# Performance work log

Hardware: AMD Instinct MI355X
Metric: run time of the kernel (lower is better)

## Reference

```python
import jax, jax.numpy as jnp
import numpy as np

B, T, C = 2, 2048, 1024
N_HEAD = 16
HEAD_DIM = C // N_HEAD


def setup_inputs() -> dict:
    key = jax.random.key(0)
    k1, k2, k3 = jax.random.split(key, 3)
    s = 1.0 / np.sqrt(C)
    return {
        "x": jax.random.normal(k1, (B, T, C), dtype=jnp.float32),
        "w_qkv": jax.random.normal(k2, (C, 3 * C), dtype=jnp.float32) * s,
        "b_qkv": jnp.zeros((3 * C,), dtype=jnp.float32),
        "w_out": jax.random.normal(k3, (C, C), dtype=jnp.float32) * s,
        "b_out": jnp.zeros((C,), dtype=jnp.float32),
    }


def reference(x, w_qkv, b_qkv, w_out, b_out):
    b, t, c = x.shape
    qkv = x @ w_qkv + b_qkv                                   # [B,T,3C]
    # Faithful to torch: view(B,T,H,3*hd).transpose(1,2) then split last dim
    qkv = qkv.reshape(b, t, N_HEAD, 3 * HEAD_DIM).transpose(0, 2, 1, 3)  # [B,H,T,3hd]
    q, k, v = jnp.split(qkv, 3, axis=-1)                      # each [B,H,T,hd]
    att = jnp.einsum("bhqd,bhkd->bhqk", q, k) / np.sqrt(HEAD_DIM)
    causal = jnp.tril(jnp.ones((t, t), dtype=bool))
    att = jnp.where(causal[None, None], att, -jnp.inf)
    att = jax.nn.softmax(att, axis=-1)                        # dropout p=0 (eval)
    y = jnp.einsum("bhqk,bhkd->bhqd", att, v)                 # [B,H,T,hd]
    y = y.transpose(0, 2, 1, 3).reshape(b, t, c)
    return y @ w_out + b_out
```

## Files before the change

kernel.cpp:

```cpp
#include <hip/hip_runtime.h>


#define T_SEQ 2048
#define C_DIM 1024
#define NH    16
#define HD    64
#define BT    4096

typedef short bf16x8 __attribute__((ext_vector_type(8)));
typedef float floatx4 __attribute__((ext_vector_type(4)));

static __device__ __forceinline__ unsigned short f2bf(float f) {
    union { float f; unsigned u; } v; v.f = f;
    unsigned u = v.u;
    return (unsigned short)((u + 0x7FFFu + ((u >> 16) & 1u)) >> 16);
}

static __device__ __forceinline__ void gl2lds16(const void* g, void* l) {
    __builtin_amdgcn_global_load_lds(
        (const __attribute__((address_space(1))) unsigned int*)g,
        (__attribute__((address_space(3))) unsigned int*)l, 16, 0, 0);
}

__global__ __launch_bounds__(256) void convert_bf16(const float* __restrict__ in,
                                                    unsigned short* __restrict__ out, int n) {
    int i = (blockIdx.x * 256 + threadIdx.x) * 4;
    const int stride = gridDim.x * 1024;
    for (; i < n; i += stride) {
        float4 f = *(const float4*)(in + i);
        ushort4 o;
        o.x = f2bf(f.x); o.y = f2bf(f.y); o.z = f2bf(f.z); o.w = f2bf(f.w);
        *(ushort4*)(out + i) = o;
    }
}

__global__ __launch_bounds__(256) void transpose_bf16(const float* __restrict__ W,
                                                      unsigned short* __restrict__ Wt,
                                                      int K, int N) {
    __shared__ float tile[64][65];
    const int k0 = blockIdx.y << 6;
    const int n0 = blockIdx.x << 6;
    const int rr = threadIdx.x >> 4;
    const int cc = (threadIdx.x & 15) << 2;
#pragma unroll
    for (int i = 0; i < 4; i++) {
        int r = rr + (i << 4);
        *(float4*)&tile[r][cc] = *(const float4*)(W + (size_t)(k0 + r) * N + n0 + cc);
    }
    __syncthreads();
#pragma unroll
    for (int i = 0; i < 4; i++) {
        int nr = rr + (i << 4);
        ushort4 o;
        o.x = f2bf(tile[cc + 0][nr]);
        o.y = f2bf(tile[cc + 1][nr]);
        o.z = f2bf(tile[cc + 2][nr]);
        o.w = f2bf(tile[cc + 3][nr]);
        *(ushort4*)(Wt + (size_t)(n0 + nr) * K + k0 + cc) = o;
    }
}

#define GEMM_CORE(A_, Bt_, K_)                                                      \
    __shared__ short As[128 * 64];                                                  \
    __shared__ short Bs[128 * 64];                                                  \
    const int tid  = threadIdx.x;                                                   \
    const int lane = tid & 63, wave = tid >> 6;                                     \
    const int ln   = lane & 15, quad = lane >> 4;                                   \
    const int wm   = wave & 1,  wn   = wave >> 1;                                   \
    const int row0 = blockIdx.y << 7;                                               \
    const int col0 = blockIdx.x << 7;                                               \
    const int trow = tid >> 3;                                                      \
    const int tcol = (tid & 7) << 3;                                                \
    floatx4 acc[4][4];                                                              \
    _Pragma("unroll")                                                               \
    for (int i = 0; i < 4; i++)                                                     \
        _Pragma("unroll")                                                           \
        for (int j = 0; j < 4; j++) acc[i][j] = (floatx4){0.f, 0.f, 0.f, 0.f};      \
    for (int k0 = 0; k0 < K_; k0 += 64) {                                           \
        _Pragma("unroll")                                                           \
        for (int i = 0; i < 4; i++) {                                               \
            int r = trow + (i << 5);                                                \
            gl2lds16(A_  + (size_t)(row0 + r) * K_ + k0 + tcol, &As[(r << 6) + tcol]); \
            gl2lds16(Bt_ + (size_t)(col0 + r) * K_ + k0 + tcol, &Bs[(r << 6) + tcol]); \
        }                                                                           \
        __syncthreads();                                                            \
        _Pragma("unroll")                                                           \
        for (int half = 0; half < 2; half++) {                                      \
            bf16x8 af[4], bfr[4];                                                   \
            _Pragma("unroll")                                                       \
            for (int t4 = 0; t4 < 4; t4++) {                                        \
                af[t4]  = *(bf16x8*)&As[(((wm << 6) + (t4 << 4) + ln) << 6) + (half << 5) + (quad << 3)]; \
                bfr[t4] = *(bf16x8*)&Bs[(((wn << 6) + (t4 << 4) + ln) << 6) + (half << 5) + (quad << 3)]; \
            }                                                                       \
            _Pragma("unroll")                                                       \
            for (int mt = 0; mt < 4; mt++)                                          \
                _Pragma("unroll")                                                   \
                for (int nt = 0; nt < 4; nt++)                                      \
                    acc[mt][nt] = __builtin_amdgcn_mfma_f32_16x16x32_bf16(af[mt], bfr[nt], acc[mt][nt], 0, 0, 0); \
        }                                                                           \
        __syncthreads();                                                            \
    }

__global__ __launch_bounds__(256) void gemm_qkv(const unsigned short* __restrict__ A,
                                                const unsigned short* __restrict__ Bt,
                                                const float* __restrict__ bias,
                                                unsigned short* __restrict__ qb,
                                                unsigned short* __restrict__ kb,
                                                unsigned short* __restrict__ vt) {
    GEMM_CORE(A, Bt, 1024)
#pragma unroll
    for (int mt = 0; mt < 4; mt++) {
#pragma unroll
        for (int nt = 0; nt < 4; nt++) {
            int n = col0 + (wn << 6) + (nt << 4) + ln;
            int h = n / 192, r = n % 192;
            int sel = r >> 6, d = r & 63;
            float bv = bias[n];
#pragma unroll
            for (int e = 0; e < 4; e++) {
                int m = row0 + (wm << 6) + (mt << 4) + (quad << 2) + e;
                int b = m >> 11, t = m & 2047;
                float val = acc[mt][nt][e] + bv;
                int bh = b * NH + h;
                if (sel == 0)
                    qb[((size_t)bh * T_SEQ + t) * HD + d] = f2bf(val * 0.125f);
                else if (sel == 1)
                    kb[((size_t)bh * T_SEQ + t) * HD + d] = f2bf(val);
                else
                    vt[((size_t)bh * HD + d) * T_SEQ + t] = f2bf(val);
            }
        }
    }
}

__global__ __launch_bounds__(256) void gemm_out(const unsigned short* __restrict__ A,
                                                const unsigned short* __restrict__ Bt,
                                                const float* __restrict__ bias,
                                                float* __restrict__ out) {
    GEMM_CORE(A, Bt, 1024)
    const int N = 1024;
#pragma unroll
    for (int mt = 0; mt < 4; mt++) {
#pragma unroll
        for (int nt = 0; nt < 4; nt++) {
            int n = col0 + (wn << 6) + (nt << 4) + ln;
            float bv = bias[n];
#pragma unroll
            for (int e = 0; e < 4; e++) {
                int m = row0 + (wm << 6) + (mt << 4) + (quad << 2) + e;
                out[(size_t)m * N + n] = acc[mt][nt][e] + bv;
            }
        }
    }
}

__global__ __launch_bounds__(256, 4) void attn(const unsigned short* __restrict__ qb,
                                               const unsigned short* __restrict__ kb,
                                               const unsigned short* __restrict__ vt,
                                               unsigned short* __restrict__ y) {
    __shared__ short Ks[64][72];
    __shared__ short Vs[64][72];
    __shared__ short QP[64][72];
    const int tid  = threadIdx.x;
    const int w    = tid >> 6, lane = tid & 63;
    const int ln   = lane & 15, quad = lane >> 4;
    const int qt   = 31 - (int)blockIdx.x;
    const int bh   = blockIdx.y;
    const size_t base = (size_t)bh * T_SEQ * HD;
    const int q0   = qt << 6;
    const int sb   = q0 + (w << 4);
    const float NEG_INF = -__builtin_inff();

    const int sr = tid >> 3;
    const int sc = (tid & 7) << 3;

    bf16x8 qtmp[2], kreg[2], vreg[2];
#pragma unroll
    for (int i = 0; i < 2; i++) {
        qtmp[i] = *(const bf16x8*)(qb + base + (size_t)(q0 + sr + (i << 5)) * HD + sc);
        kreg[i] = *(const bf16x8*)(kb + base + (size_t)(sr + (i << 5)) * HD + sc);
        vreg[i] = *(const bf16x8*)(vt + base + (size_t)(sr + (i << 5)) * T_SEQ + sc);
    }
#pragma unroll
    for (int i = 0; i < 2; i++) *(bf16x8*)&QP[sr + (i << 5)][sc] = qtmp[i];
    __syncthreads();

    bf16x8 bq0 = *(bf16x8*)&QP[(w << 4) + ln][quad << 3];
    bf16x8 bq1 = *(bf16x8*)&QP[(w << 4) + ln][32 + (quad << 3)];

    floatx4 o[4];
#pragma unroll
    for (int nt = 0; nt < 4; nt++) o[nt] = (floatx4){0.f, 0.f, 0.f, 0.f};
    float m_prev = NEG_INF, l_run = 0.f;

    for (int kt = 0; kt <= qt; kt++) {
        const int k0 = kt << 6;
        __syncthreads();
#pragma unroll
        for (int i = 0; i < 2; i++) {
            *(bf16x8*)&Ks[sr + (i << 5)][sc] = kreg[i];
            *(bf16x8*)&Vs[sr + (i << 5)][sc] = vreg[i];
        }
        __syncthreads();
        if (kt < qt) {
            const int kn = k0 + 64;
#pragma unroll
            for (int i = 0; i < 2; i++) {
                kreg[i] = *(const bf16x8*)(kb + base + (size_t)(kn + sr + (i << 5)) * HD + sc);
                vreg[i] = *(const bf16x8*)(vt + base + (size_t)(sr + (i << 5)) * T_SEQ + kn + sc);
            }
        }

        const bool diag  = (kt == qt);
        const int  nlive = diag ? w : 3;

        floatx4 st[4];
#pragma unroll
        for (int ktl = 0; ktl < 4; ktl++) {
            if (ktl <= nlive) {
                bf16x8 a0 = *(bf16x8*)&Ks[(ktl << 4) + ln][quad << 3];
                bf16x8 a1 = *(bf16x8*)&Ks[(ktl << 4) + ln][32 + (quad << 3)];
                floatx4 acc = (floatx4){0.f, 0.f, 0.f, 0.f};
                acc = __builtin_amdgcn_mfma_f32_16x16x32_bf16(a0, bq0, acc, 0, 0, 0);
                acc = __builtin_amdgcn_mfma_f32_16x16x32_bf16(a1, bq1, acc, 0, 0, 0);
                st[ktl] = acc;
            }
        }
        if (diag) {
#pragma unroll
            for (int ktl = 0; ktl < 4; ktl++) {
                if (ktl <= nlive) {
#pragma unroll
                    for (int e = 0; e < 4; e++) {
                        int kg = k0 + (ktl << 4) + (quad << 2) + e;
                        if (kg > sb + ln) st[ktl][e] = NEG_INF;
                    }
                }
            }
        }

        float mx = NEG_INF;
#pragma unroll
        for (int ktl = 0; ktl < 4; ktl++)
            if (ktl <= nlive) {
#pragma unroll
                for (int e = 0; e < 4; e++) mx = fmaxf(mx, st[ktl][e]);
            }
        mx = fmaxf(mx, __shfl_xor(mx, 16));
        mx = fmaxf(mx, __shfl_xor(mx, 32));
        float m_new = fmaxf(m_prev, mx);
        float alpha = __expf(m_prev - m_new);
        float psum = 0.f;
#pragma unroll
        for (int ktl = 0; ktl < 4; ktl++)
            if (ktl <= nlive) {
#pragma unroll
                for (int e = 0; e < 4; e++) {
                    float p = __expf(st[ktl][e] - m_new);
                    st[ktl][e] = p;
                    psum += p;
                }
            }
        psum += __shfl_xor(psum, 16);
        psum += __shfl_xor(psum, 32);
        l_run = l_run * alpha + psum;
        m_prev = m_new;

#pragma unroll
        for (int ktl = 0; ktl < 4; ktl++) {
            ushort4 pw;
            if (ktl <= nlive) {
                pw.x = f2bf(st[ktl][0]); pw.y = f2bf(st[ktl][1]);
                pw.z = f2bf(st[ktl][2]); pw.w = f2bf(st[ktl][3]);
            } else {
                pw.x = 0; pw.y = 0; pw.z = 0; pw.w = 0;
            }
            *(ushort4*)&QP[(w << 4) + ln][(ktl << 4) + (quad << 2)] = pw;
        }

        float arow[4];
#pragma unroll
        for (int e = 0; e < 4; e++) arow[e] = __shfl(alpha, (quad << 2) + e);
#pragma unroll
        for (int nt = 0; nt < 4; nt++)
#pragma unroll
            for (int e = 0; e < 4; e++) o[nt][e] *= arow[e];

        bf16x8 ap0 = *(bf16x8*)&QP[(w << 4) + ln][quad << 3];
        bf16x8 ap1 = *(bf16x8*)&QP[(w << 4) + ln][32 + (quad << 3)];
#pragma unroll
        for (int nt = 0; nt < 4; nt++) {
            bf16x8 v0 = *(bf16x8*)&Vs[(nt << 4) + ln][quad << 3];
            bf16x8 v1 = *(bf16x8*)&Vs[(nt << 4) + ln][32 + (quad << 3)];
            o[nt] = __builtin_amdgcn_mfma_f32_16x16x32_bf16(ap0, v0, o[nt], 0, 0, 0);
            o[nt] = __builtin_amdgcn_mfma_f32_16x16x32_bf16(ap1, v1, o[nt], 0, 0, 0);
        }
    }

    float linv[4];
#pragma unroll
    for (int e = 0; e < 4; e++) linv[e] = 1.0f / __shfl(l_run, (quad << 2) + e);
    const int b = bh >> 4, h = bh & 15;
#pragma unroll
    for (int e = 0; e < 4; e++) {
        int t = sb + (quad << 2) + e;
        unsigned short* yrow = y + ((size_t)b * T_SEQ + t) * C_DIM + h * HD;
#pragma unroll
        for (int nt = 0; nt < 4; nt++)
            yrow[(nt << 4) + ln] = f2bf(o[nt][e] * linv[e]);
    }
}

extern "C" void kernel_launch(void* const* d_in, const int* in_sizes, int n_in,
                              void* d_out, int out_size, void* d_ws, size_t ws_size,
                              hipStream_t stream) {
    (void)in_sizes; (void)n_in; (void)out_size; (void)ws_size;
    const float* x     = (const float*)d_in[0];
    const float* w_qkv = (const float*)d_in[1];
    const float* b_qkv = (const float*)d_in[2];
    const float* w_out = (const float*)d_in[3];
    const float* b_out = (const float*)d_in[4];
    float* out = (float*)d_out;

    char* ws = (char*)d_ws;
    unsigned short* qb    = (unsigned short*)ws;
    unsigned short* kb    = (unsigned short*)(ws + ((size_t)8  << 20));
    unsigned short* vt    = (unsigned short*)(ws + ((size_t)16 << 20));
    unsigned short* xb    = (unsigned short*)(ws + ((size_t)24 << 20));
    unsigned short* yb    = xb;
    unsigned short* wqkvT = (unsigned short*)(ws + ((size_t)32 << 20));
    unsigned short* woutT = (unsigned short*)(ws + ((size_t)38 << 20));

    convert_bf16  <<<1024, 256, 0, stream>>>(x, xb, BT * C_DIM);
    transpose_bf16<<<dim3(48, 16), 256, 0, stream>>>(w_qkv, wqkvT, 1024, 3072);
    transpose_bf16<<<dim3(16, 16), 256, 0, stream>>>(w_out, woutT, 1024, 1024);
    gemm_qkv      <<<dim3(24, 32), 256, 0, stream>>>(xb, wqkvT, b_qkv, qb, kb, vt);
    attn          <<<dim3(32, 32), 256, 0, stream>>>(qb, kb, vt, yb);
    gemm_out      <<<dim3(8, 32), 256, 0, stream>>>(yb, woutT, b_out, out);
}
```

Baseline: 245.5 us.

## Fuse prep kernels into one launch and XOR-swizzle GEMM LDS tiles

Merges the x conversion and the two weight transposes into a single prep kernel with a block-index dispatch, removing two kernel launches and their serialization. It also applies an XOR swizzle to the 16-byte chunks that global_load_lds writes into the GEMM shared-memory tiles, with matching swizzled fragment reads, to reduce LDS bank conflicts on the bf16x8 loads. The swizzle changes which global chunk each thread fetches, so it relies on the read and write index maps staying consistent.

After: 235.5 us. -4.1%, faster.

```diff
diff --git a/kernel.cpp b/kernel.cpp
--- a/kernel.cpp
+++ b/kernel.cpp
@@ -22,24 +22,12 @@
         (__attribute__((address_space(3))) unsigned int*)l, 16, 0, 0);
 }
 
-__global__ __launch_bounds__(256) void convert_bf16(const float* __restrict__ in,
-                                                    unsigned short* __restrict__ out, int n) {
-    int i = (blockIdx.x * 256 + threadIdx.x) * 4;
-    const int stride = gridDim.x * 1024;
-    for (; i < n; i += stride) {
-        float4 f = *(const float4*)(in + i);
-        ushort4 o;
-        o.x = f2bf(f.x); o.y = f2bf(f.y); o.z = f2bf(f.z); o.w = f2bf(f.w);
-        *(ushort4*)(out + i) = o;
-    }
-}
-
-__global__ __launch_bounds__(256) void transpose_bf16(const float* __restrict__ W,
+static __device__ __forceinline__ void transpose_body(float (*tile)[65],
+                                                      const float* __restrict__ W,
                                                       unsigned short* __restrict__ Wt,
-                                                      int K, int N) {
-    __shared__ float tile[64][65];
-    const int k0 = blockIdx.y << 6;
-    const int n0 = blockIdx.x << 6;
+                                                      int K, int N, int bx, int by) {
+    const int k0 = by << 6;
+    const int n0 = bx << 6;
     const int rr = threadIdx.x >> 4;
     const int cc = (threadIdx.x & 15) << 2;
 #pragma unroll
@@ -57,6 +45,33 @@
         o.z = f2bf(tile[cc + 2][nr]);
         o.w = f2bf(tile[cc + 3][nr]);
         *(ushort4*)(Wt + (size_t)(n0 + nr) * K + k0 + cc) = o;
+    }
+}
+
+__global__ __launch_bounds__(256) void prep(const float* __restrict__ x,
+                                            unsigned short* __restrict__ xb,
+                                            const float* __restrict__ w_qkv,
+                                            unsigned short* __restrict__ wqkvT,
+                                            const float* __restrict__ w_out,
+                                            unsigned short* __restrict__ woutT) {
+    __shared__ float tile[64][65];
+    const int bx = blockIdx.x;
+    if (bx < 1024) {
+        int i = (bx * 256 + threadIdx.x) * 4;
+        const int n = BT * C_DIM;
+        const int stride = 1024 * 1024;
+        for (; i < n; i += stride) {
+            float4 f = *(const float4*)(x + i);
+            ushort4 o;
+            o.x = f2bf(f.x); o.y = f2bf(f.y); o.z = f2bf(f.z); o.w = f2bf(f.w);
+            *(ushort4*)(xb + i) = o;
+        }
+    } else if (bx < 1024 + 768) {
+        int b = bx - 1024;
+        transpose_body(tile, w_qkv, wqkvT, 1024, 3072, b % 48, b / 48);
+    } else {
+        int b = bx - 1024 - 768;
+        transpose_body(tile, w_out, woutT, 1024, 1024, b % 16, b / 16);
     }
 }
 
@@ -69,8 +84,6 @@
     const int wm   = wave & 1,  wn   = wave >> 1;                                   \
     const int row0 = blockIdx.y << 7;                                               \
     const int col0 = blockIdx.x << 7;                                               \
-    const int trow = tid >> 3;                                                      \
-    const int tcol = (tid & 7) << 3;                                                \
     floatx4 acc[4][4];                                                              \
     _Pragma("unroll")                                                               \
     for (int i = 0; i < 4; i++)                                                     \
@@ -79,9 +92,11 @@
     for (int k0 = 0; k0 < K_; k0 += 64) {                                           \
         _Pragma("unroll")                                                           \
         for (int i = 0; i < 4; i++) {                                               \
-            int r = trow + (i << 5);                                                \
-            gl2lds16(A_  + (size_t)(row0 + r) * K_ + k0 + tcol, &As[(r << 6) + tcol]); \
-            gl2lds16(Bt_ + (size_t)(col0 + r) * K_ + k0 + tcol, &Bs[(r << 6) + tcol]); \
+            int c = (i << 8) + tid;                                                 \
+            int r = c >> 3;                                                         \
+            int gsrc = (c & 7) ^ (r & 7);                                           \
+            gl2lds16(A_  + (size_t)(row0 + r) * K_ + k0 + (gsrc << 3), &As[c << 3]); \
+            gl2lds16(Bt_ + (size_t)(col0 + r) * K_ + k0 + (gsrc << 3), &Bs[c << 3]); \
         }                                                                           \
         __syncthreads();                                                            \
         _Pragma("unroll")                                                           \
@@ -89,8 +104,11 @@
             bf16x8 af[4], bfr[4];                                                   \
             _Pragma("unroll")                                                       \
             for (int t4 = 0; t4 < 4; t4++) {                                        \
-                af[t4]  = *(bf16x8*)&As[(((wm << 6) + (t4 << 4) + ln) << 6) + (half << 5) + (quad << 3)]; \
-                bfr[t4] = *(bf16x8*)&Bs[(((wn << 6) + (t4 << 4) + ln) << 6) + (half << 5) + (quad << 3)]; \
+                int ra = (wm << 6) + (t4 << 4) + ln;                                \
+                int rb = (wn << 6) + (t4 << 4) + ln;                                \
+                int g  = (half << 2) + quad;                                        \
+                af[t4]  = *(bf16x8*)&As[((ra << 3) + (g ^ (ra & 7))) << 3];         \
+                bfr[t4] = *(bf16x8*)&Bs[((rb << 3) + (g ^ (rb & 7))) << 3];         \
             }                                                                       \
             _Pragma("unroll")                                                       \
             for (int mt = 0; mt < 4; mt++)                                          \
@@ -331,10 +349,8 @@
     unsigned short* wqkvT = (unsigned short*)(ws + ((size_t)32 << 20));
     unsigned short* woutT = (unsigned short*)(ws + ((size_t)38 << 20));
 
-    convert_bf16  <<<1024, 256, 0, stream>>>(x, xb, BT * C_DIM);
-    transpose_bf16<<<dim3(48, 16), 256, 0, stream>>>(w_qkv, wqkvT, 1024, 3072);
-    transpose_bf16<<<dim3(16, 16), 256, 0, stream>>>(w_out, woutT, 1024, 1024);
-    gemm_qkv      <<<dim3(24, 32), 256, 0, stream>>>(xb, wqkvT, b_qkv, qb, kb, vt);
-    attn          <<<dim3(32, 32), 256, 0, stream>>>(qb, kb, vt, yb);
-    gemm_out      <<<dim3(8, 32), 256, 0, stream>>>(yb, woutT, b_out, out);
-}
+    prep    <<<2048, 256, 0, stream>>>(x, xb, w_qkv, wqkvT, w_out, woutT);
+    gemm_qkv<<<dim3(24, 32), 256, 0, stream>>>(xb, wqkvT, b_qkv, qb, kb, vt);
+    attn    <<<dim3(32, 32), 256, 0, stream>>>(qb, kb, vt, yb);
+    gemm_out<<<dim3(8, 32), 256, 0, stream>>>(yb, woutT, b_out, out);
+}
```
